# Optimization experiments

Measured on AMD Instinct MI355X. Metric: run time of the kernel, lower is better.

The kernel has to match this reference:

```python
import jax, jax.numpy as jnp
import numpy as np

N_NODES = 100000
NEG_SLOPE = 0.2


def leaky_relu(x):
    return jnp.where(x >= 0, x, NEG_SLOPE * x)


def gat_conv(x, src, dst, W, a_src, a_dst, b, heads, out_ch, concat):
    # x: [N, F_in]; src/dst: [E]; W: [F_in, heads*out_ch]
    n = x.shape[0]
    h = (x @ W).reshape(n, heads, out_ch)                      # [N, H, C]
    s_src = jnp.einsum('nhc,hc->nh', h, a_src)                 # [N, H]
    s_dst = jnp.einsum('nhc,hc->nh', h, a_dst)                 # [N, H]
    e = leaky_relu(s_src[src] + s_dst[dst])                    # [E, H]
    # segment softmax over incoming edges of each dst node
    m = jax.ops.segment_max(e, dst, num_segments=n)            # [N, H]
    m = jnp.where(jnp.isfinite(m), m, 0.0)
    p = jnp.exp(e - m[dst])                                    # [E, H]
    denom = jax.ops.segment_sum(p, dst, num_segments=n)        # [N, H]
    alpha = p / denom[dst]                                     # [E, H]
    out = jax.ops.segment_sum(h[src] * alpha[..., None], dst, num_segments=n)  # [N, H, C]
    if concat:
        out = out.reshape(n, heads * out_ch)
    else:
        out = out.mean(axis=1)
    return out + b


def setup_inputs() -> dict:
    key = jax.random.key(0)
    ks = jax.random.split(key, 10)
    F_in, hidden, heads, n_cls = 128, 32, 8, 40
    n_edges = 1600000
    x = jax.random.normal(ks[0], (N_NODES, F_in), dtype=jnp.float32)
    edge_index = jax.random.randint(ks[1], (2, n_edges), 0, N_NODES, dtype=jnp.int64)
    s = 0.1
    W1 = jax.random.normal(ks[2], (F_in, heads * hidden), dtype=jnp.float32) * s
    att_src1 = jax.random.normal(ks[3], (heads, hidden), dtype=jnp.float32) * s
    att_dst1 = jax.random.normal(ks[4], (heads, hidden), dtype=jnp.float32) * s
    b1 = jnp.zeros((heads * hidden,), dtype=jnp.float32)
    W2 = jax.random.normal(ks[5], (heads * hidden, n_cls), dtype=jnp.float32) * s
    att_src2 = jax.random.normal(ks[6], (1, n_cls), dtype=jnp.float32) * s
    att_dst2 = jax.random.normal(ks[7], (1, n_cls), dtype=jnp.float32) * s
    b2 = jnp.zeros((n_cls,), dtype=jnp.float32)
    return {
        'x': x, 'edge_index': edge_index,
        'W1': W1, 'att_src1': att_src1, 'att_dst1': att_dst1, 'b1': b1,
        'W2': W2, 'att_src2': att_src2, 'att_dst2': att_dst2, 'b2': b2,
    }


def reference(x, edge_index, W1, att_src1, att_dst1, b1, W2, att_src2, att_dst2, b2):
    n = x.shape[0]
    # PyG GATConv default: add self loops
    loop = jnp.arange(n, dtype=edge_index.dtype)
    src = jnp.concatenate([edge_index[0], loop])
    dst = jnp.concatenate([edge_index[1], loop])
    h = gat_conv(x, src, dst, W1, att_src1, att_dst1, b1, heads=8, out_ch=32, concat=True)
    h = jax.nn.relu(h)  # dropout p=0 / eval mode: identity
    out = gat_conv(h, src, dst, W2, att_src2, att_dst2, b2, heads=1, out_ch=40, concat=True)
    return jax.nn.log_softmax(out, axis=1)
```

## Files before the change

kernel.cpp:

```cpp
#include <hip/hip_runtime.h>
#include <hip/hip_bf16.h>
#include <cmath>


typedef unsigned short ushortT;
typedef unsigned int uintT;
typedef unsigned char ucharT;
typedef __attribute__((ext_vector_type(8))) short short8;
typedef __attribute__((ext_vector_type(4))) float float4v;
typedef __attribute__((ext_vector_type(2))) float float2v;

static __device__ __forceinline__ float bflo(uintT u) {
    return __uint_as_float(u << 16);
}
static __device__ __forceinline__ float bfhi(uintT u) {
    return __uint_as_float(u & 0xffff0000u);
}
static __device__ __forceinline__ ushortT f2bf(float f) {
    __hip_bfloat16 h = __float2bfloat16(f);
    return *reinterpret_cast<ushortT*>(&h);
}
static __device__ __forceinline__ uintT pk(float a, float b) {
    return (uintT)f2bf(a) | ((uintT)f2bf(b) << 16);
}
static __device__ __forceinline__ float ub(uintT u, int k) {
    return (float)((u >> (8 * k)) & 0xffu);
}
static __device__ __forceinline__ float lrelu(float e) {
    return 0.6f * e + 0.4f * fabsf(e);
}

#define PREP_BLOCKS 184
#define EPB 4096

__global__ __launch_bounds__(256) void k_prep(const float* __restrict__ W1,
                                              const float* __restrict__ W2,
                                              const float* __restrict__ a1s,
                                              const float* __restrict__ a1d,
                                              ushortT* __restrict__ W1t,
                                              ushortT* __restrict__ W2t) {
    int t = blockIdx.x * 256 + threadIdx.x;
    if (t < 128 * 256) {
        int k = t >> 8, s = t & 255;
        int c = ((s & 15) << 4) | (s >> 4);
        W1t[s * 128 + k] = f2bf(W1[(size_t)k * 256 + c]);
    } else if (t < 128 * 256 + 48 * 256) {
        int q = t - 128 * 256;
        int k = q / 48, c = q - k * 48;
        W2t[c * 256 + k] = (c < 40) ? f2bf(W2[k * 40 + c]) : (ushortT)0;
    } else if (t < 128 * 256 + 48 * 256 + 2048) {
        int q = t - (128 * 256 + 48 * 256);
        int k = q >> 4, j = q & 15;
        int h = j & 7;
        const float* av = ((j < 8) ? a1s : a1d) + h * 32;
        const float* wr = W1 + (size_t)k * 256 + h * 32;
        float s = 0.f;
        #pragma unroll
        for (int c = 0; c < 32; ++c) s += wr[c] * av[c];
        W1t[(256 + j) * 128 + k] = f2bf(s);
    }
}

static __device__ __forceinline__ void dev_gemm1(int slab,
                                                 const float* __restrict__ A,
                                                 const ushortT* __restrict__ Bt,
                                                 ucharT* __restrict__ h1i,
                                                 float* __restrict__ s1c,
                                                 float* __restrict__ s1d, int M) {
    int lane = threadIdx.x & 63;
    int r0 = slab * 16;
    if (r0 >= M) return;
    int n = lane & 15, q = lane >> 4;
    const float* arow = A + (size_t)(r0 + n) * 128 + q * 8;
    short8 af[4];
    #pragma unroll
    for (int s = 0; s < 4; ++s) {
        float4 v0 = *(const float4*)(arow + s * 32);
        float4 v1 = *(const float4*)(arow + s * 32 + 4);
        short8 a;
        a[0] = (short)f2bf(v0.x); a[1] = (short)f2bf(v0.y);
        a[2] = (short)f2bf(v0.z); a[3] = (short)f2bf(v0.w);
        a[4] = (short)f2bf(v1.x); a[5] = (short)f2bf(v1.y);
        a[6] = (short)f2bf(v1.z); a[7] = (short)f2bf(v1.w);
        af[s] = a;
    }
    float4v acc[17];
    #pragma unroll
    for (int j = 0; j < 17; ++j) acc[j] = (float4v){0.f, 0.f, 0.f, 0.f};
    #pragma unroll
    for (int s = 0; s < 4; ++s) {
        #pragma unroll
        for (int j = 0; j < 17; ++j) {
            short8 b = *(const short8*)(Bt + (size_t)(j * 16 + n) * 128 + s * 32 + q * 8);
            acc[j] = __builtin_amdgcn_mfma_f32_16x16x32_bf16(af[s], b, acc[j], 0, 0, 0);
        }
    }
    float am[4];
    #pragma unroll
    for (int r = 0; r < 4; ++r) {
        float m = 0.f;
        #pragma unroll
        for (int j = 0; j < 16; ++j) m = fmaxf(m, fabsf(acc[j][r]));
        am[r] = m;
    }
    #pragma unroll
    for (int off = 1; off < 16; off <<= 1) {
        #pragma unroll
        for (int r = 0; r < 4; ++r) am[r] = fmaxf(am[r], __shfl_xor(am[r], off, 64));
    }
    #pragma unroll
    for (int r = 0; r < 4; ++r) {
        int row = r0 + q * 4 + r;
        float m = am[r];
        float si = (m > 0.f) ? 127.f / m : 0.f;
        uintT wd[4];
        #pragma unroll
        for (int wq = 0; wq < 4; ++wq) {
            uintT p4 = 0;
            #pragma unroll
            for (int b = 0; b < 4; ++b) {
                int j = wq * 4 + b;
                int qv = (int)rintf(acc[j][r] * si) + 128;
                p4 |= ((uintT)(qv & 0xff)) << (8 * b);
            }
            wd[wq] = p4;
        }
        uint4 o = make_uint4(wd[0], wd[1], wd[2], wd[3]);
        *(uint4*)(h1i + (size_t)row * 256 + n * 16) = o;
        if (n == 0) s1c[(size_t)row * 9 + 8] = m * (1.f / 127.f);
        float vv = acc[16][r];
        if (n < 8) s1c[(size_t)row * 9 + n] = vv;
        else       s1d[(size_t)row * 8 + (n - 8)] = vv;
    }
}

__global__ __launch_bounds__(256) void k_cnt_g1(const int* __restrict__ ei, int E,
                                                int* __restrict__ counts, int nbuck,
                                                const float* __restrict__ A,
                                                const ushortT* __restrict__ Bt,
                                                ucharT* __restrict__ h1i,
                                                float* __restrict__ s1c,
                                                float* __restrict__ s1d,
                                                int M, int nPrim, int slabBase) {
    if (blockIdx.x >= nPrim) {
        int wave = threadIdx.x >> 6;
        int slab = slabBase + (blockIdx.x - nPrim) * 4 + wave;
        dev_gemm1(slab, A, Bt, h1i, s1c, s1d, M);
        return;
    }
    __shared__ int h[1024];
    int t = threadIdx.x;
    for (int i = t; i < nbuck; i += 256) h[i] = 0;
    __syncthreads();
    int base = blockIdx.x * EPB;
    #pragma unroll
    for (int r = 0; r < 4; ++r) {
        int i4 = base + (r * 256 + t) * 4;
        if (i4 + 3 < E) {
            int4 d = *(const int4*)(ei + E + i4);
            atomicAdd(&h[d.x >> 7], 1);
            atomicAdd(&h[d.y >> 7], 1);
            atomicAdd(&h[d.z >> 7], 1);
            atomicAdd(&h[d.w >> 7], 1);
        } else {
            for (int j = i4; j < E; ++j) atomicAdd(&h[ei[E + j] >> 7], 1);
        }
    }
    __syncthreads();
    int* crow = counts + (size_t)blockIdx.x * nbuck;
    for (int i = t; i < nbuck; i += 256) crow[i] = h[i];
}

__global__ __launch_bounds__(256) void k_scan_cols(int* __restrict__ counts,
                                                   int* __restrict__ totals,
                                                   int nb1, int nbuck) {
    __shared__ int wsum[4];
    int k = blockIdx.x;
    int t = threadIdx.x, lane = t & 63, wv = t >> 6;
    int e0 = 2 * t, e1 = 2 * t + 1;
    int v0 = (e0 < nb1) ? counts[(size_t)e0 * nbuck + k] : 0;
    int v1 = (e1 < nb1) ? counts[(size_t)e1 * nbuck + k] : 0;
    int s = v0 + v1;
    int incl = s;
    #pragma unroll
    for (int off = 1; off < 64; off <<= 1) {
        int u = __shfl_up(incl, off, 64);
        if (lane >= off) incl += u;
    }
    if (lane == 63) wsum[wv] = incl;
    __syncthreads();
    int add = 0;
    if (wv > 0) add += wsum[0];
    if (wv > 1) add += wsum[1];
    if (wv > 2) add += wsum[2];
    incl += add;
    int excl = incl - s;
    if (e0 < nb1) counts[(size_t)e0 * nbuck + k] = excl;
    if (e1 < nb1) counts[(size_t)e1 * nbuck + k] = excl + v0;
    if (t == 255) totals[k] = incl;
}

__global__ __launch_bounds__(256) void k_place_g1(const int* __restrict__ ei, int E,
                                                  const int* __restrict__ counts,
                                                  const int* __restrict__ totals,
                                                  int* __restrict__ bstart,
                                                  uintT* __restrict__ tmp, int nbuck,
                                                  const float* __restrict__ A,
                                                  const ushortT* __restrict__ Bt,
                                                  ucharT* __restrict__ h1i,
                                                  float* __restrict__ s1c,
                                                  float* __restrict__ s1d,
                                                  int M, int nPrim, int slabBase) {
    if (blockIdx.x >= nPrim) {
        int wave = threadIdx.x >> 6;
        int slab = slabBase + (blockIdx.x - nPrim) * 4 + wave;
        dev_gemm1(slab, A, Bt, h1i, s1c, s1d, M);
        return;
    }
    __shared__ int st[1024];
    __shared__ int pos[1024];
    __shared__ int wsum[4];
    int t = threadIdx.x, lane = t & 63, wv = t >> 6;
    int b = blockIdx.x;
    int g[4];
    int s = 0;
    #pragma unroll
    for (int j = 0; j < 4; ++j) {
        int e = 4 * t + j;
        g[j] = (e < nbuck) ? totals[e] : 0;
        s += g[j];
    }
    int incl = s;
    #pragma unroll
    for (int off = 1; off < 64; off <<= 1) {
        int u = __shfl_up(incl, off, 64);
        if (lane >= off) incl += u;
    }
    if (lane == 63) wsum[wv] = incl;
    __syncthreads();
    int add = 0;
    if (wv > 0) add += wsum[0];
    if (wv > 1) add += wsum[1];
    if (wv > 2) add += wsum[2];
    int excl = incl + add - s;
    #pragma unroll
    for (int j = 0; j < 4; ++j) {
        int e = 4 * t + j;
        if (e < nbuck) st[e] = excl;
        excl += g[j];
    }
    __syncthreads();
    const int* crow = counts + (size_t)b * nbuck;
    for (int i = t; i < nbuck; i += 256) {
        int sv = st[i];
        pos[i] = sv + crow[i];
        if (b == 0) bstart[i] = sv;
    }
    __syncthreads();
    int base = b * EPB;
    #pragma unroll
    for (int r = 0; r < 4; ++r) {
        int i4 = base + (r * 256 + t) * 4;
        if (i4 + 3 < E) {
            int4 sv = *(const int4*)(ei + i4);
            int4 dv = *(const int4*)(ei + E + i4);
            int p0 = atomicAdd(&pos[dv.x >> 7], 1);
            tmp[p0] = (uintT)sv.x | (((uintT)dv.x & 127u) << 17);
            int p1 = atomicAdd(&pos[dv.y >> 7], 1);
            tmp[p1] = (uintT)sv.y | (((uintT)dv.y & 127u) << 17);
            int p2 = atomicAdd(&pos[dv.z >> 7], 1);
            tmp[p2] = (uintT)sv.z | (((uintT)dv.z & 127u) << 17);
            int p3 = atomicAdd(&pos[dv.w >> 7], 1);
            tmp[p3] = (uintT)sv.w | (((uintT)dv.w & 127u) << 17);
        } else {
            for (int j = i4; j < E; ++j) {
                int sj = ei[j], dj = ei[E + j];
                int p = atomicAdd(&pos[dj >> 7], 1);
                tmp[p] = (uintT)sj | (((uintT)dj & 127u) << 17);
            }
        }
    }
}

__global__ __launch_bounds__(256) void k_csr_g1(const uintT* __restrict__ tmp,
                                                const int* __restrict__ bstart,
                                                const int* __restrict__ totals,
                                                int* __restrict__ rowptr,
                                                int* __restrict__ csr_src,
                                                int N, int nbuck,
                                                const float* __restrict__ A,
                                                const ushortT* __restrict__ Bt,
                                                ucharT* __restrict__ h1i,
                                                float* __restrict__ s1c,
                                                float* __restrict__ s1d,
                                                int M, int nPrim, int slabBase) {
    if (blockIdx.x >= nPrim) {
        int wave = threadIdx.x >> 6;
        int slab = slabBase + (blockIdx.x - nPrim) * 4 + wave;
        dev_gemm1(slab, A, Bt, h1i, s1c, s1d, M);
        return;
    }
    __shared__ int cnt[128];
    __shared__ int cur[128];
    __shared__ int wtot;
    int k = blockIdx.x;
    int t = threadIdx.x;
    int nodeBase = k << 7;
    int nn = N - nodeBase;
    if (nn > 128) nn = 128;
    int myStart = bstart[k];
    int myCount = totals[k];
    int csrBase = myStart + nodeBase;
    if (t < 128) cnt[t] = 0;
    __syncthreads();
    for (int i = t; i < myCount; i += 256) {
        uintT p = tmp[myStart + i];
        atomicAdd(&cnt[p >> 17], 1);
    }
    __syncthreads();
    int dseg = 0, incl = 0;
    if (t < 128) {
        dseg = (t < nn) ? cnt[t] + 1 : 0;
        incl = dseg;
        #pragma unroll
        for (int off = 1; off < 64; off <<= 1) {
            int u = __shfl_up(incl, off, 64);
            if ((t & 63) >= off) incl += u;
        }
        if (t == 63) wtot = incl;
    }
    __syncthreads();
    if (t < nn) {
        int excl = incl - dseg + ((t >= 64) ? wtot : 0);
        int rp = csrBase + excl;
        int node = nodeBase + t;
        rowptr[node + 1] = rp + dseg;
        csr_src[rp] = node;
        cur[t] = rp + 1;
    }
    if (k == 0 && t == 0) rowptr[0] = 0;
    __syncthreads();
    for (int i = t; i < myCount; i += 256) {
        uintT p = tmp[myStart + i];
        int ld = p >> 17;
        int q = atomicAdd(&cur[ld], 1);
        csr_src[q] = (int)(p & 0x1FFFFu);
    }
}

struct Edge1 {
    float sv, sc;
    uint4 v;
    int si;
};

static __device__ __forceinline__ void ldi1(Edge1& S, int j, int endm1,
                                            const int* __restrict__ csr_src) {
    int jj = j < endm1 ? j : endm1;
    S.si = csr_src[jj];
}

static __device__ __forceinline__ void ldv1(Edge1& S, int j, int end,
                                            const float* __restrict__ s1c,
                                            const ucharT* __restrict__ hb, int head) {
    if (j < end) {
        int s = S.si;
        const float* sb = s1c + (size_t)s * 9;
        S.sv = sb[head];
        S.sc = sb[8];
        S.v = *(const uint4*)(hb + (size_t)s * 256);
    }
}

static __device__ __forceinline__ void ac1(const Edge1& S, float sdn,
                                           float2v* A, float& l, float& sps) {
    float p = __expf(lrelu(S.sv + sdn));
    l += p;
    float ps = p * S.sc;
    sps += ps;
    float2v p2 = {ps, ps};
    uintT w;
    w = S.v.x;
    A[0] += p2 * (float2v){ub(w, 0), ub(w, 1)};
    A[1] += p2 * (float2v){ub(w, 2), ub(w, 3)};
    w = S.v.y;
    A[2] += p2 * (float2v){ub(w, 0), ub(w, 1)};
    A[3] += p2 * (float2v){ub(w, 2), ub(w, 3)};
    w = S.v.z;
    A[4] += p2 * (float2v){ub(w, 0), ub(w, 1)};
    A[5] += p2 * (float2v){ub(w, 2), ub(w, 3)};
    w = S.v.w;
    A[6] += p2 * (float2v){ub(w, 0), ub(w, 1)};
    A[7] += p2 * (float2v){ub(w, 2), ub(w, 3)};
}

__global__ __launch_bounds__(256) void k_agg1(const ucharT* __restrict__ h1i,
                                              const float* __restrict__ s1c,
                                              const float* __restrict__ s1d,
                                              const int* __restrict__ rowptr,
                                              const int* __restrict__ csr_src,
                                              const float* __restrict__ b1,
                                              ushortT* __restrict__ out1, int N) {
    int lane = threadIdx.x & 63;
    int wid = threadIdx.x >> 6;
    int n = blockIdx.x * 4 + wid;
    if (n >= N) return;
    int g = lane >> 4;
    int cl = lane & 15;
    int head = cl >> 1;
    int beg = rowptr[n], end = rowptr[n + 1];
    float sdn = s1d[(size_t)n * 8 + head];
    const ucharT* hb = h1i + cl * 16;
    float2v A[8];
    #pragma unroll
    for (int k = 0; k < 8; ++k) A[k] = (float2v){0.f, 0.f};
    float l = 0.f, sps = 0.f;
    int i0 = beg + g;
    if (i0 < end) {
        int endm1 = end - 1;
        Edge1 S0, S1, S2;
        S0.sv = S1.sv = S2.sv = 0.f;
        S0.sc = S1.sc = S2.sc = 0.f;
        S0.v = S1.v = S2.v = make_uint4(0u, 0u, 0u, 0u);
        ldi1(S0, i0, endm1, csr_src);
        ldi1(S1, i0 + 4, endm1, csr_src);
        ldi1(S2, i0 + 8, endm1, csr_src);
        ldv1(S0, i0, end, s1c, hb, head);
        ldv1(S1, i0 + 4, end, s1c, hb, head);
        ldv1(S2, i0 + 8, end, s1c, hb, head);
        ldi1(S0, i0 + 12, endm1, csr_src);
        ldi1(S1, i0 + 16, endm1, csr_src);
        ldi1(S2, i0 + 20, endm1, csr_src);
        for (int idx = i0; idx < end; idx += 12) {
            ac1(S0, sdn, A, l, sps);
            ldv1(S0, idx + 12, end, s1c, hb, head);
            ldi1(S0, idx + 24, endm1, csr_src);
            if (idx + 4 < end) {
                ac1(S1, sdn, A, l, sps);
                ldv1(S1, idx + 16, end, s1c, hb, head);
                ldi1(S1, idx + 28, endm1, csr_src);
            }
            if (idx + 8 < end) {
                ac1(S2, sdn, A, l, sps);
                ldv1(S2, idx + 20, end, s1c, hb, head);
                ldi1(S2, idx + 32, endm1, csr_src);
            }
        }
    }
    #pragma unroll
    for (int off = 16; off < 64; off <<= 1) {
        l += __shfl_xor(l, off, 64);
        sps += __shfl_xor(sps, off, 64);
        #pragma unroll
        for (int k = 0; k < 8; ++k) {
            A[k].x += __shfl_xor(A[k].x, off, 64);
            A[k].y += __shfl_xor(A[k].y, off, 64);
        }
    }
    if (g == 0) {
        float inv = 1.f / l;
        float adj = 128.f * sps;
        const float4 bb0 = *(const float4*)(b1 + cl * 16);
        const float4 bb1 = *(const float4*)(b1 + cl * 16 + 4);
        const float4 bb2 = *(const float4*)(b1 + cl * 16 + 8);
        const float4 bb3 = *(const float4*)(b1 + cl * 16 + 12);
        float bbf[16] = {bb0.x, bb0.y, bb0.z, bb0.w, bb1.x, bb1.y, bb1.z, bb1.w,
                         bb2.x, bb2.y, bb2.z, bb2.w, bb3.x, bb3.y, bb3.z, bb3.w};
        uintT o[8];
        #pragma unroll
        for (int k = 0; k < 8; ++k) {
            float x0 = fmaxf((A[k].x - adj) * inv + bbf[2 * k], 0.f);
            float x1 = fmaxf((A[k].y - adj) * inv + bbf[2 * k + 1], 0.f);
            o[k] = pk(x0, x1);
        }
        *(uint4*)(out1 + (size_t)n * 256 + cl * 16) =
            make_uint4(o[0], o[1], o[2], o[3]);
        *(uint4*)(out1 + (size_t)n * 256 + cl * 16 + 8) =
            make_uint4(o[4], o[5], o[6], o[7]);
    }
}

__global__ __launch_bounds__(256) void k_gemm2(const ushortT* __restrict__ X,
                                               const ushortT* __restrict__ Bt,
                                               const float* __restrict__ a2s,
                                               const float* __restrict__ a2d,
                                               ushortT* __restrict__ H2,
                                               float* __restrict__ s2d, int M) {
    int lane = threadIdx.x & 63, wave = threadIdx.x >> 6;
    int slab = blockIdx.x * 4 + wave;
    int r0 = slab * 16;
    if (r0 >= M) return;
    int n = lane & 15, q = lane >> 4;
    const ushortT* xrow = X + (size_t)(r0 + n) * 256 + q * 8;
    float4v acc[3];
    #pragma unroll
    for (int j = 0; j < 3; ++j) acc[j] = (float4v){0.f, 0.f, 0.f, 0.f};
    #pragma unroll
    for (int s = 0; s < 8; ++s) {
        short8 a = *(const short8*)(xrow + s * 32);
        #pragma unroll
        for (int j = 0; j < 3; ++j) {
            short8 b = *(const short8*)(Bt + (size_t)(j * 16 + n) * 256 + s * 32 + q * 8);
            acc[j] = __builtin_amdgcn_mfma_f32_16x16x32_bf16(a, b, acc[j], 0, 0, 0);
        }
    }
    float asv[3], adv[3];
    #pragma unroll
    for (int j = 0; j < 3; ++j) {
        int col = j * 16 + n;
        asv[j] = (col < 40) ? a2s[col] : 0.f;
        adv[j] = (col < 40) ? a2d[col] : 0.f;
    }
    float us[4], ud[4];
    #pragma unroll
    for (int r = 0; r < 4; ++r) {
        us[r] = acc[0][r] * asv[0] + acc[1][r] * asv[1] + acc[2][r] * asv[2];
        ud[r] = acc[0][r] * adv[0] + acc[1][r] * adv[1] + acc[2][r] * adv[2];
    }
    #pragma unroll
    for (int off = 1; off < 16; off <<= 1) {
        #pragma unroll
        for (int r = 0; r < 4; ++r) {
            us[r] += __shfl_xor(us[r], off, 64);
            ud[r] += __shfl_xor(ud[r], off, 64);
        }
    }
    #pragma unroll
    for (int j = 0; j < 3; ++j) {
        int col = j * 16 + n;
        if (col < 40) {
            #pragma unroll
            for (int r = 0; r < 4; ++r)
                H2[(size_t)(r0 + q * 4 + r) * 48 + col] = f2bf(acc[j][r]);
        }
    }
    if (n == 0) {
        #pragma unroll
        for (int r = 0; r < 4; ++r) {
            int row = r0 + q * 4 + r;
            *(float*)(H2 + (size_t)row * 48 + 40) = us[r];
            s2d[row] = ud[r];
        }
    }
}

struct Edge2 {
    float sv;
    uint2 v;
    int si;
};

static __device__ __forceinline__ void ldi2(Edge2& S, int j, int endm1,
                                            const int* __restrict__ csr_src) {
    int jj = j < endm1 ? j : endm1;
    S.si = csr_src[jj];
}

static __device__ __forceinline__ void ldv2(Edge2& S, int j, int end,
                                            const ushortT* __restrict__ h2, int cl) {
    if (j < end) {
        int s = S.si;
        const ushortT* hr = h2 + (size_t)s * 48;
        S.v = *(const uint2*)(hr + cl * 4);
        S.sv = *(const float*)(hr + 40);
    }
}

static __device__ __forceinline__ void ac2(const Edge2& S, float sdn,
                                           float2v& A01, float2v& A23, float& l) {
    float p = __expf(lrelu(S.sv + sdn));
    l += p;
    float2v p2 = {p, p};
    A01 += p2 * (float2v){bflo(S.v.x), bfhi(S.v.x)};
    A23 += p2 * (float2v){bflo(S.v.y), bfhi(S.v.y)};
}

__global__ __launch_bounds__(256) void k_agg2lsm(const ushortT* __restrict__ h2,
                                                 const float* __restrict__ sd,
                                                 const int* __restrict__ rowptr,
                                                 const int* __restrict__ csr_src,
                                                 const float* __restrict__ b2,
                                                 float* __restrict__ out, int N) {
    int lane = threadIdx.x & 63;
    int wid = threadIdx.x >> 6;
    int n = blockIdx.x * 4 + wid;
    if (n >= N) return;
    int el = lane / 10;
    int cl = lane - el * 10;
    int beg = rowptr[n], end = rowptr[n + 1];
    float sdn = sd[n];
    float2v A01 = (float2v){0.f, 0.f}, A23 = (float2v){0.f, 0.f};
    float l = 0.f;
    if (el < 6) {
        int i0 = beg + el;
        if (i0 < end) {
            int endm1 = end - 1;
            Edge2 S0, S1, S2;
            S0.sv = S1.sv = S2.sv = 0.f;
            S0.v = S1.v = S2.v = make_uint2(0u, 0u);
            ldi2(S0, i0, endm1, csr_src);
            ldi2(S1, i0 + 6, endm1, csr_src);
            ldi2(S2, i0 + 12, endm1, csr_src);
            ldv2(S0, i0, end, h2, cl);
            ldv2(S1, i0 + 6, end, h2, cl);
            ldv2(S2, i0 + 12, end, h2, cl);
            ldi2(S0, i0 + 18, endm1, csr_src);
            ldi2(S1, i0 + 24, endm1, csr_src);
            ldi2(S2, i0 + 30, endm1, csr_src);
            for (int idx = i0; idx < end; idx += 18) {
                ac2(S0, sdn, A01, A23, l);
                ldv2(S0, idx + 18, end, h2, cl);
                ldi2(S0, idx + 36, endm1, csr_src);
                if (idx + 6 < end) {
                    ac2(S1, sdn, A01, A23, l);
                    ldv2(S1, idx + 24, end, h2, cl);
                    ldi2(S1, idx + 42, endm1, csr_src);
                }
                if (idx + 12 < end) {
                    ac2(S2, sdn, A01, A23, l);
                    ldv2(S2, idx + 30, end, h2, cl);
                    ldi2(S2, idx + 48, endm1, csr_src);
                }
            }
        }
    }
    float a0 = A01.x, a1 = A01.y, a2 = A23.x, a3 = A23.y;
    float t0 = 0.f, t1 = 0.f, t2 = 0.f, t3 = 0.f, lt = 0.f;
    #pragma unroll
    for (int k = 0; k < 6; ++k) {
        int sl = cl + 10 * k;
        t0 += __shfl(a0, sl, 64);
        t1 += __shfl(a1, sl, 64);
        t2 += __shfl(a2, sl, 64);
        t3 += __shfl(a3, sl, 64);
        if (cl == 0) lt += __shfl(l, sl, 64);
    }
    lt = __shfl(lt, 0, 64);
    float inv = 1.f / lt;
    float o0 = t0 * inv + b2[cl * 4 + 0];
    float o1 = t1 * inv + b2[cl * 4 + 1];
    float o2 = t2 * inv + b2[cl * 4 + 2];
    float o3 = t3 * inv + b2[cl * 4 + 3];
    float lm = (lane < 10) ? fmaxf(fmaxf(o0, o1), fmaxf(o2, o3)) : -INFINITY;
    #pragma unroll
    for (int off = 32; off; off >>= 1) lm = fmaxf(lm, __shfl_xor(lm, off, 64));
    float le = (lane < 10)
        ? __expf(o0 - lm) + __expf(o1 - lm) + __expf(o2 - lm) + __expf(o3 - lm)
        : 0.f;
    #pragma unroll
    for (int off = 32; off; off >>= 1) le += __shfl_xor(le, off, 64);
    float ls = lm + logf(le);
    if (lane < 10) {
        float4 w = make_float4(o0 - ls, o1 - ls, o2 - ls, o3 - ls);
        *(float4*)(out + (size_t)n * 40 + cl * 4) = w;
    }
}

extern "C" void kernel_launch(void* const* d_in, const int* in_sizes, int n_in,
                              void* d_out, int out_size, void* d_ws, size_t ws_size,
                              hipStream_t stream) {
    const float* x   = (const float*)d_in[0];
    const int*   ei  = (const int*)d_in[1];
    const float* W1  = (const float*)d_in[2];
    const float* a1s = (const float*)d_in[3];
    const float* a1d = (const float*)d_in[4];
    const float* b1  = (const float*)d_in[5];
    const float* W2  = (const float*)d_in[6];
    const float* a2s = (const float*)d_in[7];
    const float* a2d = (const float*)d_in[8];
    const float* b2  = (const float*)d_in[9];
    float* out = (float*)d_out;

    const int N = in_sizes[0] / 128;
    const int E = in_sizes[1] / 2;
    const int ET = E + N;
    const int NBUCK = (N + 127) >> 7;
    const int NB1 = (E + EPB - 1) / EPB;

    char* w = (char*)d_ws;
    ucharT* h1i = (ucharT*)w;
    ushortT* out1b = (ushortT*)(w + (size_t)N * 256);
    int* i_row = (int*)(w + (size_t)N * 768);
    float* s1c = (float*)(w + (size_t)N * 768 + ((size_t)N + 16) * 4);
    float* s1d = s1c + (size_t)N * 9;
    int* i_cnt = (int*)(s1d + (size_t)N * 8);
    int* i_tot = i_cnt + (size_t)NB1 * NBUCK;
    int* i_bst = i_tot + NBUCK + 2;
    uintT* i_tmp = (uintT*)(i_bst + NBUCK + 2);
    int* i_csr = (int*)(i_tmp + E);
    ushortT* W1t = (ushortT*)(i_csr + ET);
    ushortT* W2t = W1t + 272 * 128;
    ushortT* h2b = (ushortT*)s1c;
    float* s2d = (float*)(i_tmp + (size_t)(E - N - 16));

    const int nb4 = (N + 3) / 4;
    const int nbG = (N / 16 + 3) / 4;
    const int CH  = (nbG + 2) / 3;

    k_prep<<<PREP_BLOCKS, 256, 0, stream>>>(W1, W2, a1s, a1d, W1t, W2t);
    k_cnt_g1<<<NB1 + CH, 256, 0, stream>>>(ei, E, i_cnt, NBUCK,
                                           x, W1t, h1i, s1c, s1d,
                                           N, NB1, 0);
    k_scan_cols<<<NBUCK, 256, 0, stream>>>(i_cnt, i_tot, NB1, NBUCK);
    k_place_g1<<<NB1 + CH, 256, 0, stream>>>(ei, E, i_cnt, i_tot, i_bst, i_tmp, NBUCK,
                                             x, W1t, h1i, s1c, s1d,
                                             N, NB1, CH * 4);
    k_csr_g1<<<NBUCK + CH, 256, 0, stream>>>(i_tmp, i_bst, i_tot, i_row, i_csr,
                                             N, NBUCK,
                                             x, W1t, h1i, s1c, s1d,
                                             N, NBUCK, CH * 8);

    k_agg1<<<nb4, 256, 0, stream>>>(h1i, s1c, s1d, i_row, i_csr, b1, out1b, N);

    k_gemm2<<<nbG, 256, 0, stream>>>(out1b, W2t, a2s, a2d, h2b, s2d, N);
    k_agg2lsm<<<nb4, 256, 0, stream>>>(h2b, s2d, i_row, i_csr, b2, out, N);
}
```

Before: 400.1 us.

## Split CSR build in halves and overlap second half with layer-1 aggregation

The CSR construction is split by bucket halves: the first half runs alongside the GEMM1 tail, and the second half runs in the same launch as aggregation of the first half of nodes, followed by a separate aggregation launch for the rest. The per-node score and scale are interleaved into float2 pairs so each edge needs one 8-byte load instead of two scalar loads. Attention coefficients are prescaled by log2(e) so exp2f replaces __expf. These changes add a kernel launch and a 16-float-per-node layout, and they depend on the fact that the first half of nodes only needs the first half of the CSR.

```diff
diff --git a/kernel.cpp b/kernel.cpp
--- a/kernel.cpp
+++ b/kernel.cpp
@@ -9,6 +9,8 @@
 typedef __attribute__((ext_vector_type(8))) short short8;
 typedef __attribute__((ext_vector_type(4))) float float4v;
 typedef __attribute__((ext_vector_type(2))) float float2v;
+
+#define LOG2E 1.4426950408889634f
 
 static __device__ __forceinline__ float bflo(uintT u) {
     return __uint_as_float(u << 16);
@@ -57,7 +59,7 @@
         float s = 0.f;
         #pragma unroll
         for (int c = 0; c < 32; ++c) s += wr[c] * av[c];
-        W1t[(256 + j) * 128 + k] = f2bf(s);
+        W1t[(256 + j) * 128 + k] = f2bf(s * LOG2E);
     }
 }
 
@@ -65,7 +67,7 @@
                                                  const float* __restrict__ A,
                                                  const ushortT* __restrict__ Bt,
                                                  ucharT* __restrict__ h1i,
-                                                 float* __restrict__ s1c,
+                                                 float* __restrict__ s1cc,
                                                  float* __restrict__ s1d, int M) {
     int lane = threadIdx.x & 63;
     int r0 = slab * 16;
@@ -127,10 +129,13 @@
         }
         uint4 o = make_uint4(wd[0], wd[1], wd[2], wd[3]);
         *(uint4*)(h1i + (size_t)row * 256 + n * 16) = o;
-        if (n == 0) s1c[(size_t)row * 9 + 8] = m * (1.f / 127.f);
         float vv = acc[16][r];
-        if (n < 8) s1c[(size_t)row * 9 + n] = vv;
-        else       s1d[(size_t)row * 8 + (n - 8)] = vv;
+        if (n < 8) {
+            *(float2*)(s1cc + ((size_t)row << 4) + n * 2) =
+                make_float2(vv, m * (1.f / 127.f));
+        } else {
+            s1d[(size_t)row * 8 + (n - 8)] = vv;
+        }
     }
 }
 
@@ -139,13 +144,13 @@
                                                 const float* __restrict__ A,
                                                 const ushortT* __restrict__ Bt,
                                                 ucharT* __restrict__ h1i,
-                                                float* __restrict__ s1c,
+                                                float* __restrict__ s1cc,
                                                 float* __restrict__ s1d,
                                                 int M, int nPrim, int slabBase) {
     if (blockIdx.x >= nPrim) {
         int wave = threadIdx.x >> 6;
         int slab = slabBase + (blockIdx.x - nPrim) * 4 + wave;
-        dev_gemm1(slab, A, Bt, h1i, s1c, s1d, M);
+        dev_gemm1(slab, A, Bt, h1i, s1cc, s1d, M);
         return;
     }
     __shared__ int h[1024];
@@ -208,13 +213,13 @@
                                                   const float* __restrict__ A,
                                                   const ushortT* __restrict__ Bt,
                                                   ucharT* __restrict__ h1i,
-                                                  float* __restrict__ s1c,
+                                                  float* __restrict__ s1cc,
                                                   float* __restrict__ s1d,
                                                   int M, int nPrim, int slabBase) {
     if (blockIdx.x >= nPrim) {
         int wave = threadIdx.x >> 6;
         int slab = slabBase + (blockIdx.x - nPrim) * 4 + wave;
-        dev_gemm1(slab, A, Bt, h1i, s1c, s1d, M);
+        dev_gemm1(slab, A, Bt, h1i, s1cc, s1d, M);
         return;
     }
     __shared__ int st[1024];
@@ -282,28 +287,14 @@
     }
 }
 
-__global__ __launch_bounds__(256) void k_csr_g1(const uintT* __restrict__ tmp,
-                                                const int* __restrict__ bstart,
-                                                const int* __restrict__ totals,
-                                                int* __restrict__ rowptr,
-                                                int* __restrict__ csr_src,
-                                                int N, int nbuck,
-                                                const float* __restrict__ A,
-                                                const ushortT* __restrict__ Bt,
-                                                ucharT* __restrict__ h1i,
-                                                float* __restrict__ s1c,
-                                                float* __restrict__ s1d,
-                                                int M, int nPrim, int slabBase) {
-    if (blockIdx.x >= nPrim) {
-        int wave = threadIdx.x >> 6;
-        int slab = slabBase + (blockIdx.x - nPrim) * 4 + wave;
-        dev_gemm1(slab, A, Bt, h1i, s1c, s1d, M);
-        return;
-    }
-    __shared__ int cnt[128];
-    __shared__ int cur[128];
-    __shared__ int wtot;
-    int k = blockIdx.x;
+static __device__ __forceinline__ void dev_csr(int k,
+                                               const uintT* __restrict__ tmp,
+                                               const int* __restrict__ bstart,
+                                               const int* __restrict__ totals,
+                                               int* __restrict__ rowptr,
+                                               int* __restrict__ csr_src,
+                                               int N, int* cnt, int* cur,
+                                               int* wtot) {
     int t = threadIdx.x;
     int nodeBase = k << 7;
     int nn = N - nodeBase;
@@ -327,11 +318,11 @@
             int u = __shfl_up(incl, off, 64);
             if ((t & 63) >= off) incl += u;
         }
-        if (t == 63) wtot = incl;
+        if (t == 63) *wtot = incl;
     }
     __syncthreads();
     if (t < nn) {
-        int excl = incl - dseg + ((t >= 64) ? wtot : 0);
+        int excl = incl - dseg + ((t >= 64) ? *wtot : 0);
         int rp = csrBase + excl;
         int node = nodeBase + t;
         rowptr[node + 1] = rp + dseg;
@@ -348,8 +339,32 @@
     }
 }
 
+__global__ __launch_bounds__(256) void k_csr_g1(const uintT* __restrict__ tmp,
+                                                const int* __restrict__ bstart,
+                                                const int* __restrict__ totals,
+                                                int* __restrict__ rowptr,
+                                                int* __restrict__ csr_src,
+                                                int N,
+                                                const float* __restrict__ A,
+                                                const ushortT* __restrict__ Bt,
+                                                ucharT* __restrict__ h1i,
+                                                float* __restrict__ s1cc,
+                                                float* __restrict__ s1d,
+                                                int M, int nPrim, int slabBase) {
+    __shared__ int cnt[128];
+    __shared__ int cur[128];
+    __shared__ int wtot;
+    if (blockIdx.x >= nPrim) {
+        int wave = threadIdx.x >> 6;
+        int slab = slabBase + (blockIdx.x - nPrim) * 4 + wave;
+        dev_gemm1(slab, A, Bt, h1i, s1cc, s1d, M);
+        return;
+    }
+    dev_csr(blockIdx.x, tmp, bstart, totals, rowptr, csr_src, N, cnt, cur, &wtot);
+}
+
 struct Edge1 {
-    float sv, sc;
+    float2 svc;
     uint4 v;
     int si;
 };
@@ -361,22 +376,20 @@
 }
 
 static __device__ __forceinline__ void ldv1(Edge1& S, int j, int end,
-                                            const float* __restrict__ s1c,
+                                            const float2* __restrict__ sc2,
                                             const ucharT* __restrict__ hb, int head) {
     if (j < end) {
         int s = S.si;
-        const float* sb = s1c + (size_t)s * 9;
-        S.sv = sb[head];
-        S.sc = sb[8];
-        S.v = *(const uint4*)(hb + (size_t)s * 256);
+        S.svc = sc2[((size_t)s << 3) + head];
+        S.v = *(const uint4*)(hb + ((size_t)s << 8));
     }
 }
 
 static __device__ __forceinline__ void ac1(const Edge1& S, float sdn,
                                            float2v* A, float& l, float& sps) {
-    float p = __expf(lrelu(S.sv + sdn));
+    float p = exp2f(lrelu(S.svc.x + sdn));
     l += p;
-    float ps = p * S.sc;
+    float ps = p * S.svc.y;
     sps += ps;
     float2v p2 = {ps, ps};
     uintT w;
@@ -394,23 +407,22 @@
     A[7] += p2 * (float2v){ub(w, 2), ub(w, 3)};
 }
 
-__global__ __launch_bounds__(256) void k_agg1(const ucharT* __restrict__ h1i,
-                                              const float* __restrict__ s1c,
-                                              const float* __restrict__ s1d,
-                                              const int* __restrict__ rowptr,
-                                              const int* __restrict__ csr_src,
-                                              const float* __restrict__ b1,
-                                              ushortT* __restrict__ out1, int N) {
+static __device__ __forceinline__ void dev_agg1(int n,
+                                                const ucharT* __restrict__ h1i,
+                                                const float* __restrict__ s1cc,
+                                                const float* __restrict__ s1d,
+                                                const int* __restrict__ rowptr,
+                                                const int* __restrict__ csr_src,
+                                                const float* __restrict__ b1,
+                                                ushortT* __restrict__ out1) {
     int lane = threadIdx.x & 63;
-    int wid = threadIdx.x >> 6;
-    int n = blockIdx.x * 4 + wid;
-    if (n >= N) return;
     int g = lane >> 4;
     int cl = lane & 15;
     int head = cl >> 1;
     int beg = rowptr[n], end = rowptr[n + 1];
     float sdn = s1d[(size_t)n * 8 + head];
     const ucharT* hb = h1i + cl * 16;
+    const float2* sc2 = (const float2*)s1cc;
     float2v A[8];
     #pragma unroll
     for (int k = 0; k < 8; ++k) A[k] = (float2v){0.f, 0.f};
@@ -419,30 +431,29 @@
     if (i0 < end) {
         int endm1 = end - 1;
         Edge1 S0, S1, S2;
-        S0.sv = S1.sv = S2.sv = 0.f;
-        S0.sc = S1.sc = S2.sc = 0.f;
+        S0.svc = S1.svc = S2.svc = make_float2(0.f, 0.f);
         S0.v = S1.v = S2.v = make_uint4(0u, 0u, 0u, 0u);
         ldi1(S0, i0, endm1, csr_src);
         ldi1(S1, i0 + 4, endm1, csr_src);
         ldi1(S2, i0 + 8, endm1, csr_src);
-        ldv1(S0, i0, end, s1c, hb, head);
-        ldv1(S1, i0 + 4, end, s1c, hb, head);
-        ldv1(S2, i0 + 8, end, s1c, hb, head);
+        ldv1(S0, i0, end, sc2, hb, head);
+        ldv1(S1, i0 + 4, end, sc2, hb, head);
+        ldv1(S2, i0 + 8, end, sc2, hb, head);
         ldi1(S0, i0 + 12, endm1, csr_src);
         ldi1(S1, i0 + 16, endm1, csr_src);
         ldi1(S2, i0 + 20, endm1, csr_src);
         for (int idx = i0; idx < end; idx += 12) {
             ac1(S0, sdn, A, l, sps);
-            ldv1(S0, idx + 12, end, s1c, hb, head);
+            ldv1(S0, idx + 12, end, sc2, hb, head);
             ldi1(S0, idx + 24, endm1, csr_src);
             if (idx + 4 < end) {
                 ac1(S1, sdn, A, l, sps);
-                ldv1(S1, idx + 16, end, s1c, hb, head);
+                ldv1(S1, idx + 16, end, sc2, hb, head);
                 ldi1(S1, idx + 28, endm1, csr_src);
             }
             if (idx + 8 < end) {
                 ac1(S2, sdn, A, l, sps);
-                ldv1(S2, idx + 20, end, s1c, hb, head);
+                ldv1(S2, idx + 20, end, sc2, hb, head);
                 ldi1(S2, idx + 32, endm1, csr_src);
             }
         }
@@ -478,6 +489,43 @@
         *(uint4*)(out1 + (size_t)n * 256 + cl * 16 + 8) =
             make_uint4(o[4], o[5], o[6], o[7]);
     }
+}
+
+__global__ __launch_bounds__(256) void k_csr_agg1(const uintT* __restrict__ tmp,
+                                                  const int* __restrict__ bstart,
+                                                  const int* __restrict__ totals,
+                                                  int* __restrict__ rowptr,
+                                                  int* __restrict__ csr_src,
+                                                  int N, int halfB, int nP4,
+                                                  const ucharT* __restrict__ h1i,
+                                                  const float* __restrict__ s1cc,
+                                                  const float* __restrict__ s1d,
+                                                  const float* __restrict__ b1,
+                                                  ushortT* __restrict__ out1, int H) {
+    __shared__ int cnt[128];
+    __shared__ int cur[128];
+    __shared__ int wtot;
+    if (blockIdx.x < nP4) {
+        dev_csr(halfB + blockIdx.x, tmp, bstart, totals, rowptr, csr_src, N,
+                cnt, cur, &wtot);
+        return;
+    }
+    int n = (blockIdx.x - nP4) * 4 + (threadIdx.x >> 6);
+    if (n >= H) return;
+    dev_agg1(n, h1i, s1cc, s1d, rowptr, csr_src, b1, out1);
+}
+
+__global__ __launch_bounds__(256) void k_agg1(const ucharT* __restrict__ h1i,
+                                              const float* __restrict__ s1cc,
+                                              const float* __restrict__ s1d,
+                                              const int* __restrict__ rowptr,
+                                              const int* __restrict__ csr_src,
+                                              const float* __restrict__ b1,
+                                              ushortT* __restrict__ out1,
+                                              int base, int N) {
+    int n = base + blockIdx.x * 4 + (threadIdx.x >> 6);
+    if (n >= N) return;
+    dev_agg1(n, h1i, s1cc, s1d, rowptr, csr_src, b1, out1);
 }
 
 __global__ __launch_bounds__(256) void k_gemm2(const ushortT* __restrict__ X,
@@ -508,8 +556,8 @@
     #pragma unroll
     for (int j = 0; j < 3; ++j) {
         int col = j * 16 + n;
-        asv[j] = (col < 40) ? a2s[col] : 0.f;
-        adv[j] = (col < 40) ? a2d[col] : 0.f;
+        asv[j] = (col < 40) ? a2s[col] * LOG2E : 0.f;
+        adv[j] = (col < 40) ? a2d[col] * LOG2E : 0.f;
     }
     float us[4], ud[4];
     #pragma unroll
@@ -568,7 +616,7 @@
 
 static __device__ __forceinline__ void ac2(const Edge2& S, float sdn,
                                            float2v& A01, float2v& A23, float& l) {
-    float p = __expf(lrelu(S.sv + sdn));
+    float p = exp2f(lrelu(S.sv + sdn));
     l += p;
     float2v p2 = {p, p};
     A01 += p2 * (float2v){bflo(S.v.x), bfhi(S.v.x)};
@@ -681,8 +729,8 @@
     ucharT* h1i = (ucharT*)w;
     ushortT* out1b = (ushortT*)(w + (size_t)N * 256);
     int* i_row = (int*)(w + (size_t)N * 768);
-    float* s1c = (float*)(w + (size_t)N * 768 + ((size_t)N + 16) * 4);
-    float* s1d = s1c + (size_t)N * 9;
+    float* s1cc = (float*)(w + (size_t)N * 768 + ((size_t)N + 16) * 4);
+    float* s1d = s1cc + (size_t)N * 16;
     int* i_cnt = (int*)(s1d + (size_t)N * 8);
     int* i_tot = i_cnt + (size_t)NB1 * NBUCK;
     int* i_bst = i_tot + NBUCK + 2;
@@ -690,27 +738,32 @@
     int* i_csr = (int*)(i_tmp + E);
     ushortT* W1t = (ushortT*)(i_csr + ET);
     ushortT* W2t = W1t + 272 * 128;
-    ushortT* h2b = (ushortT*)s1c;
-    float* s2d = (float*)(i_tmp + (size_t)(E - N - 16));
+    ushortT* h2b = (ushortT*)s1cc;
+    float* s2d = (float*)i_cnt;
 
     const int nb4 = (N + 3) / 4;
     const int nbG = (N / 16 + 3) / 4;
     const int CH  = (nbG + 2) / 3;
+    const int halfB = NBUCK >> 1;
+    const int H = halfB << 7;
+    const int nP4b = NBUCK - halfB;
 
     k_prep<<<PREP_BLOCKS, 256, 0, stream>>>(W1, W2, a1s, a1d, W1t, W2t);
     k_cnt_g1<<<NB1 + CH, 256, 0, stream>>>(ei, E, i_cnt, NBUCK,
-                                           x, W1t, h1i, s1c, s1d,
+                                           x, W1t, h1i, s1cc, s1d,
                                            N, NB1, 0);
     k_scan_cols<<<NBUCK, 256, 0, stream>>>(i_cnt, i_tot, NB1, NBUCK);
     k_place_g1<<<NB1 + CH, 256, 0, stream>>>(ei, E, i_cnt, i_tot, i_bst, i_tmp, NBUCK,
-                                             x, W1t, h1i, s1c, s1d,
+                                             x, W1t, h1i, s1cc, s1d,
                                              N, NB1, CH * 4);
-    k_csr_g1<<<NBUCK + CH, 256, 0, stream>>>(i_tmp, i_bst, i_tot, i_row, i_csr,
-                                             N, NBUCK,
-                                             x, W1t, h1i, s1c, s1d,
-                                             N, NBUCK, CH * 8);
-
-    k_agg1<<<nb4, 256, 0, stream>>>(h1i, s1c, s1d, i_row, i_csr, b1, out1b, N);
+    k_csr_g1<<<halfB + CH, 256, 0, stream>>>(i_tmp, i_bst, i_tot, i_row, i_csr, N,
+                                             x, W1t, h1i, s1cc, s1d,
+                                             N, halfB, CH * 8);
+    k_csr_agg1<<<nP4b + H / 4, 256, 0, stream>>>(i_tmp, i_bst, i_tot, i_row, i_csr,
+                                                 N, halfB, nP4b,
+                                                 h1i, s1cc, s1d, b1, out1b, H);
+    k_agg1<<<(N - H + 3) / 4, 256, 0, stream>>>(h1i, s1cc, s1d, i_row, i_csr, b1,
+                                                out1b, H, N);
 
     k_gemm2<<<nbG, 256, 0, stream>>>(out1b, W2t, a2s, a2d, h2b, s2d, N);
     k_agg2lsm<<<nb4, 256, 0, stream>>>(h2b, s2d, i_row, i_csr, b2, out, N);
```

Result: no change. 407.1 us (+1.8%).
